# Kernel optimization log

Hardware: AMD Instinct MI355X
Metric: run time of the kernel (lower is better)

Reference implementation:

```python
import jax, jax.numpy as jnp
import numpy as np

N, E, IN, H, OUT, L = 100000, 1600000, 128, 64, 64, 3


def setup_inputs() -> dict:
    key = jax.random.key(0)
    ks = jax.random.split(key, 20)
    g = lambda i, shape: jax.random.normal(ks[i], shape, dtype=jnp.float32) * 0.05
    # architecture mixture weights: softmax of log_alpha ~ N(1, 0.01)
    sm = lambda i, rows, n: jax.nn.softmax(1.0 + 0.01 * jax.random.normal(ks[i], (rows, n), dtype=jnp.float32), axis=-1)
    return dict(
        x=jax.random.normal(ks[0], (N, IN), dtype=jnp.float32),
        edge_index=jax.random.randint(ks[1], (2, E), 0, N, dtype=jnp.int32),
        W_pre=g(2, (IN, H)), b_pre=jnp.zeros((H,), jnp.float32),
        W_self=g(3, (L, H, H)), b_self=jnp.zeros((L, H), jnp.float32),
        W_nbr=g(4, (L, H, H)), b_nbr=jnp.zeros((L, H), jnp.float32),
        W_comb=g(5, (L, 2 * H, H)), b_comb=jnp.zeros((L, H), jnp.float32),
        W_lc=g(6, (L, 2 * H, H)), b_lc=jnp.zeros((L, H), jnp.float32),
        ln_g=jnp.ones((L, H), jnp.float32), ln_b=jnp.zeros((L, H), jnp.float32),
        prelu_w=jnp.full((L,), 0.25, jnp.float32),
        W_lagg=g(7, ((L + 1) * H, H)), b_lagg=jnp.zeros((H,), jnp.float32),
        W_ff1=g(8, (H, H)), b_ff1=jnp.zeros((H,), jnp.float32),
        W_ff2=g(9, (H, OUT)), b_ff2=jnp.zeros((OUT,), jnp.float32),
        Z_agg=sm(10, L, 3), Z_comb=sm(11, L, 2), Z_act=sm(12, L, 2),
        Z_lc=sm(13, L, 3), Z_lagg=sm(14, 1, 3),
    )


def _layernorm(x, g, b, eps=1e-5):
    mu = x.mean(-1, keepdims=True)
    var = ((x - mu) ** 2).mean(-1, keepdims=True)
    return (x - mu) / jnp.sqrt(var + eps) * g + b


def reference(x, edge_index, W_pre, b_pre, W_self, b_self, W_nbr, b_nbr,
              W_comb, b_comb, W_lc, b_lc, ln_g, ln_b, prelu_w,
              W_lagg, b_lagg, W_ff1, b_ff1, W_ff2, b_ff2,
              Z_agg, Z_comb, Z_act, Z_lc, Z_lagg):
    n = x.shape[0]
    src, tgt = edge_index[0], edge_index[1]
    cnt = jax.ops.segment_sum(jnp.ones((src.shape[0], 1), x.dtype), tgt, num_segments=n)
    x = x @ W_pre + b_pre                       # preprocess: [N, H]
    embs = [x]
    for i in range(L):
        x_self = x @ W_self[i] + b_self[i]
        x_nl = x @ W_nbr[i] + b_nbr[i]
        msg = x_nl[src]                         # gather messages [E, H]
        s = jax.ops.segment_sum(msg, tgt, num_segments=n)
        mean = s / jnp.maximum(cnt, 1.0)
        mx = jax.ops.segment_max(msg, tgt, num_segments=n)
        mx = jnp.where(cnt > 0, mx, 0.0)        # empty segments -> 0 (PyG convention)
        x_n = Z_agg[i, 0] * s + Z_agg[i, 1] * mean + Z_agg[i, 2] * mx
        # combine mixture: sum / concat+merge
        c_sum = x_self + x_n
        c_cat = jnp.concatenate([x_self, x_n], -1) @ W_comb[i] + b_comb[i]
        h = Z_comb[i, 0] * c_sum + Z_comb[i, 1] * c_cat
        # act mixture: relu / prelu
        h = Z_act[i, 0] * jax.nn.relu(h) + Z_act[i, 1] * jnp.where(h > 0, h, prelu_w[i] * h)
        h = _layernorm(h, ln_g[i], ln_b[i])
        embs.append(h)
        # layer_connect mixture: stack / skip_sum / skip_cat
        lc_cat = jnp.concatenate([embs[-2], embs[-1]], -1) @ W_lc[i] + b_lc[i]
        x = Z_lc[i, 0] * h + Z_lc[i, 1] * (h + embs[-2]) + Z_lc[i, 2] * lc_cat
    # layer_agg mixture: none / max_pooling / concat+merge over emb_list
    a_none = embs[-1]
    a_max = jnp.stack(embs, 0).max(0)
    a_cat = jnp.concatenate(embs, -1) @ W_lagg + b_lagg
    out = Z_lagg[0, 0] * a_none + Z_lagg[0, 1] * a_max + Z_lagg[0, 2] * a_cat
    # feed-forward head (node-level task, no global pooling)
    out = jax.nn.relu(out @ W_ff1 + b_ff1) @ W_ff2 + b_ff2
    return out
```

## Files before the change

### kernel.cpp

```cpp
#include <hip/hip_runtime.h>

typedef unsigned short u16;
typedef unsigned int u32;
using bfrag = __attribute__((ext_vector_type(8))) short;
using f4v   = __attribute__((ext_vector_type(4))) float;

#define DIV_UP(a,b) (((a)+(b)-1)/(b))
#define PTILE 4096
#define CHB 512
#define CHSH 9
#define NBKT 256
#define MFMA(a,b,c) __builtin_amdgcn_mfma_f32_16x16x32_bf16(a,b,c,0,0,0)

__device__ inline u16 f2bf(float f){
  union { float f; u32 u; } v; v.f = f;
  u32 u = v.u;
  return (u16)((u + 0x7fffu + ((u >> 16) & 1u)) >> 16);
}
__device__ inline float bf2f(u16 h){
  union { u32 u; float f; } v; v.u = ((u32)h) << 16;
  return v.f;
}
__device__ inline bfrag ldA(const u16* A, long r, int koff, int lane){
  return *reinterpret_cast<const bfrag*>(A + r*64 + koff + ((lane>>4)<<3));
}
__device__ inline bfrag ldW(const u16* Wf, int kb, int cb, int lane){
  return *reinterpret_cast<const bfrag*>(Wf + (((kb*4+cb)*64 + lane)<<3));
}

__device__ inline void xpose_store(u16* sT, int lane, const f4v (&acc)[4]){
  const int cl = lane & 15, g = lane >> 4;
#pragma unroll
  for (int j = 0; j < 4; ++j){
    const int lr = g*4 + j;
#pragma unroll
    for (int cb = 0; cb < 4; ++cb){
      const int colblk = cb*2 + (cl >> 3);
      const int gr = colblk ^ (lr & 7);
      sT[lr*64 + gr*8 + (cl & 7)] = f2bf(acc[cb][j]);
    }
  }
}
__device__ inline bfrag xpose_load(const u16* sT, int lane, int kb){
  const int row = lane & 15, colblk = kb*4 + (lane >> 4);
  const int gr = colblk ^ (row & 7);
  return *reinterpret_cast<const bfrag*>(sT + row*64 + gr*8);
}

__global__ void initBkt_k(int* __restrict__ bktCnt, int bstride){
  if (threadIdx.x < NBKT) bktCnt[threadIdx.x] = threadIdx.x * bstride;
}
__global__ void partition_k(const int* __restrict__ tgt, const int* __restrict__ src,
                            int E, int* __restrict__ bktCnt, int2* __restrict__ bkt){
  __shared__ int hist[NBKT], base[NBKT], pos[NBKT];
  const int t = threadIdx.x;
  hist[t] = 0;
  __syncthreads();
  const int e0 = blockIdx.x * PTILE;
  const int e1 = (e0 + PTILE < E) ? e0 + PTILE : E;
  for (int i = e0 + t; i < e1; i += NBKT)
    atomicAdd(&hist[tgt[i] >> CHSH], 1);
  __syncthreads();
  base[t] = (hist[t] > 0) ? atomicAdd(&bktCnt[t], hist[t]) : 0;
  pos[t] = 0;
  __syncthreads();
  for (int i = e0 + t; i < e1; i += NBKT){
    int tv = tgt[i], sv = src[i];
    int c = tv >> CHSH;
    int p = base[c] + atomicAdd(&pos[c], 1);
    bkt[p] = make_int2(tv, sv);
  }
}

__global__ __launch_bounds__(CHB) void sortChunk_k(const int2* __restrict__ bkt,
    const int* __restrict__ bktCnt, int bstride, int N,
    int* __restrict__ cnt, int* __restrict__ off, int* __restrict__ perm){
  __shared__ int hist[CHB], sbase[CHB];
  const int c = blockIdx.x, t = threadIdx.x;
  const int lo = c * CHB;
  const int s = c * bstride, e = bktCnt[c];
  hist[t] = 0;
  __syncthreads();
  for (int i = s + t; i < e; i += CHB)
    atomicAdd(&hist[bkt[i].x - lo], 1);
  __syncthreads();
  const int v = hist[t];
  for (int o = 1; o < CHB; o <<= 1){
    int add = (t >= o) ? hist[t - o] : 0;
    __syncthreads();
    hist[t] += add;
    __syncthreads();
  }
  const int excl = hist[t] - v;
  if (lo + t < N){ cnt[lo + t] = v; off[lo + t] = s + excl; }
  sbase[t] = s + excl;
  __syncthreads();
  hist[t] = 0;
  __syncthreads();
  for (int i = s + t; i < e; i += CHB){
    int2 ed = bkt[i];
    int r = ed.x - lo;
    int p = sbase[r] + atomicAdd(&hist[r], 1);
    perm[p] = ed.y;
  }
}

__global__ void matW_k(const float* __restrict__ W_self, const float* __restrict__ W_comb,
                       const float* __restrict__ b_self,
                       float* __restrict__ WsWct, float* __restrict__ bsWct){
  const int b = blockIdx.x;
  const int i = b / 65, r = b % 65;
  const int c = threadIdx.x;
  const float* Wc = W_comb + i*8192;
  float s = 0.f;
  if (r < 64){
    const float* a = W_self + i*4096 + r*64;
#pragma unroll 8
    for (int k = 0; k < 64; ++k) s += a[k] * Wc[k*64 + c];
    WsWct[i*4096 + r*64 + c] = s;
  } else {
    const float* a = b_self + i*64;
#pragma unroll 8
    for (int k = 0; k < 64; ++k) s += a[k] * Wc[k*64 + c];
    bsWct[i*64 + c] = s;
  }
}

__global__ void buildAll_k(const float* __restrict__ W_self, const float* __restrict__ W_comb,
    const float* __restrict__ b_self, const float* __restrict__ b_comb,
    const float* __restrict__ Z_comb, const float* __restrict__ WsWct,
    const float* __restrict__ bsWct,
    const float* __restrict__ W_lc, const float* __restrict__ b_lc,
    const float* __restrict__ Z_lc,
    const float* __restrict__ W_lagg, const float* __restrict__ b_lagg,
    const float* __restrict__ Z_lagg,
    float* __restrict__ W1eff, float* __restrict__ W2eff, float* __restrict__ beff,
    float* __restrict__ Wlceff, float* __restrict__ blceff,
    float* __restrict__ Wle, float* __restrict__ ble){
  int idx = blockIdx.x*blockDim.x + threadIdx.x;
  if (idx < 12288){
    int i = idx >> 12, rem = idx & 4095, k = rem >> 6, c = rem & 63;
    float zc0 = Z_comb[i*2], zc1 = Z_comb[i*2+1];
    W1eff[idx] = zc0*W_self[idx] + zc1*WsWct[idx];
    W2eff[idx] = (k == c ? zc0 : 0.f) + zc1*W_comb[i*8192 + (64 + k)*64 + c];
    return;
  }
  idx -= 12288;
  if (idx < 16384){
    int i = idx >> 13, rem = idx & 8191, k = rem >> 6, c = rem & 63;
    float z0 = Z_lc[i*3], z1 = Z_lc[i*3+1], z2 = Z_lc[i*3+2];
    float idv = (k < 64) ? (k == c ? z1 : 0.f) : ((k - 64) == c ? (z0 + z1) : 0.f);
    Wlceff[idx] = z2*W_lc[idx] + idv;
    return;
  }
  idx -= 16384;
  if (idx < 20480){
    int k = idx >> 6, c = idx & 63;
    float v = (k < 256) ? Z_lagg[2]*W_lagg[idx] : 0.f;
    if (k >= 192 && k < 256 && (k - 192) == c) v += Z_lagg[0];
    if (k >= 256 && (k - 256) == c) v += Z_lagg[1];
    Wle[idx] = v;
    return;
  }
  idx -= 20480;
  if (idx < 192){
    int i = idx >> 6;
    float zc0 = Z_comb[i*2], zc1 = Z_comb[i*2+1];
    beff[idx] = zc0*b_self[idx] + zc1*(bsWct[idx] + b_comb[idx]);
    return;
  }
  idx -= 192;
  if (idx < 128){
    int i = idx >> 6;
    blceff[idx] = Z_lc[i*3+2]*b_lc[idx];
    return;
  }
  idx -= 128;
  if (idx < 64) ble[idx] = Z_lagg[2]*b_lagg[idx];
}

struct PackJobs {
  const float* src[15];
  u16* dst[15];
  int nkb[15];
};
__global__ void pack_all_k(PackJobs pj){
  const int job = blockIdx.x >> 4, kb = blockIdx.x & 15;
  if (kb >= pj.nkb[job]) return;
  const int t = threadIdx.x, cb = t >> 6, lane = t & 63;
  const float* S = pj.src[job];
  u16* D = pj.dst[job] + (((kb*4 + cb)*64 + lane) << 3);
  const int kbase = kb*32 + ((lane >> 4) << 3), c = cb*16 + (lane & 15);
#pragma unroll
  for (int j = 0; j < 8; ++j) D[j] = f2bf(S[(kbase + j)*64 + c]);
}

__global__ __launch_bounds__(256) void gemmP_k(const float* __restrict__ X,
    const u16* __restrict__ Wf, const float* __restrict__ bias,
    const u16* __restrict__ Wn, const float* __restrict__ bn,
    u16* __restrict__ out, u16* __restrict__ xnl, int N){
  __shared__ u16 sT[4][1024];
  const int lane = threadIdx.x & 63, w = threadIdx.x >> 6;
  const int R = blockIdx.x*64 + w*16;
  bfrag wf[4][4], wn[2][4];
#pragma unroll
  for (int kb = 0; kb < 4; ++kb)
#pragma unroll
    for (int cb = 0; cb < 4; ++cb) wf[kb][cb] = ldW(Wf, kb, cb, lane);
#pragma unroll
  for (int kb = 0; kb < 2; ++kb)
#pragma unroll
    for (int cb = 0; cb < 4; ++cb) wn[kb][cb] = ldW(Wn, kb, cb, lane);
  float bv[4], bnv[4];
#pragma unroll
  for (int cb = 0; cb < 4; ++cb){ bv[cb] = bias[cb*16 + (lane & 15)]; bnv[cb] = bn[cb*16 + (lane & 15)]; }
  const long ra = (R + (lane & 15) < N) ? (R + (lane & 15)) : (N - 1);
  f4v acc[4] = {f4v{0,0,0,0}, f4v{0,0,0,0}, f4v{0,0,0,0}, f4v{0,0,0,0}};
#pragma unroll
  for (int kb = 0; kb < 4; ++kb){
    const float* ap = X + ra*128 + kb*32 + ((lane >> 4) << 3);
    float4 q0 = *reinterpret_cast<const float4*>(ap);
    float4 q1 = *reinterpret_cast<const float4*>(ap + 4);
    bfrag a;
    a[0] = (short)f2bf(q0.x); a[1] = (short)f2bf(q0.y);
    a[2] = (short)f2bf(q0.z); a[3] = (short)f2bf(q0.w);
    a[4] = (short)f2bf(q1.x); a[5] = (short)f2bf(q1.y);
    a[6] = (short)f2bf(q1.z); a[7] = (short)f2bf(q1.w);
#pragma unroll
    for (int cb = 0; cb < 4; ++cb) acc[cb] = MFMA(a, wf[kb][cb], acc[cb]);
  }
#pragma unroll
  for (int cb = 0; cb < 4; ++cb)
#pragma unroll
    for (int j = 0; j < 4; ++j) acc[cb][j] += bv[cb];
  const int rbase = R + ((lane >> 4) << 2), cl = lane & 15;
#pragma unroll
  for (int cb = 0; cb < 4; ++cb)
#pragma unroll
    for (int j = 0; j < 4; ++j){
      int r = rbase + j;
      if (r < N) out[(size_t)r*64 + cb*16 + cl] = f2bf(acc[cb][j]);
    }
  xpose_store(sT[w], lane, acc);
  f4v ac2[4] = {f4v{0,0,0,0}, f4v{0,0,0,0}, f4v{0,0,0,0}, f4v{0,0,0,0}};
#pragma unroll
  for (int kb = 0; kb < 2; ++kb){
    bfrag a = xpose_load(sT[w], lane, kb);
#pragma unroll
    for (int cb = 0; cb < 4; ++cb) ac2[cb] = MFMA(a, wn[kb][cb], ac2[cb]);
  }
#pragma unroll
  for (int cb = 0; cb < 4; ++cb)
#pragma unroll
    for (int j = 0; j < 4; ++j){
      int r = rbase + j;
      if (r < N) xnl[(size_t)r*64 + cb*16 + cl] = f2bf(ac2[cb][j] + bnv[cb]);
    }
}

__global__ __launch_bounds__(256) void gemmC_k(const u16* __restrict__ A1,
    const u16* __restrict__ A2, const u16* __restrict__ Wf1, const u16* __restrict__ Wf2,
    const float* __restrict__ beff, const float* __restrict__ lng, const float* __restrict__ lnb,
    const float* __restrict__ Zact, const float* __restrict__ prelu,
    u16* __restrict__ out, int N){
  const int lane = threadIdx.x & 63, w = threadIdx.x >> 6;
  const int R = blockIdx.x*64 + w*16;
  bfrag wf1[2][4], wf2[2][4];
#pragma unroll
  for (int kb = 0; kb < 2; ++kb)
#pragma unroll
    for (int cb = 0; cb < 4; ++cb){ wf1[kb][cb] = ldW(Wf1, kb, cb, lane); wf2[kb][cb] = ldW(Wf2, kb, cb, lane); }
  float bv[4], lgv[4], lbv[4];
#pragma unroll
  for (int cb = 0; cb < 4; ++cb){
    int c = cb*16 + (lane & 15);
    bv[cb] = beff[c]; lgv[cb] = lng[c]; lbv[cb] = lnb[c];
  }
  const float zt0 = Zact[0], zt1 = Zact[1], pw = prelu[0];
  const long ra = (R + (lane & 15) < N) ? (R + (lane & 15)) : (N - 1);
  f4v acc[4] = {f4v{0,0,0,0}, f4v{0,0,0,0}, f4v{0,0,0,0}, f4v{0,0,0,0}};
#pragma unroll
  for (int kb = 0; kb < 2; ++kb){
    bfrag a = ldA(A1, ra, kb*32, lane);
#pragma unroll
    for (int cb = 0; cb < 4; ++cb) acc[cb] = MFMA(a, wf1[kb][cb], acc[cb]);
  }
#pragma unroll
  for (int kb = 0; kb < 2; ++kb){
    bfrag a = ldA(A2, ra, kb*32, lane);
#pragma unroll
    for (int cb = 0; cb < 4; ++cb) acc[cb] = MFMA(a, wf2[kb][cb], acc[cb]);
  }
#pragma unroll
  for (int cb = 0; cb < 4; ++cb)
#pragma unroll
    for (int j = 0; j < 4; ++j){
      float v = acc[cb][j] + bv[cb];
      v = zt0*fmaxf(v, 0.f) + zt1*((v > 0.f) ? v : pw*v);
      acc[cb][j] = v;
    }
  const int rbase = R + ((lane >> 4) << 2), cl = lane & 15;
#pragma unroll
  for (int j = 0; j < 4; ++j){
    float s = acc[0][j] + acc[1][j] + acc[2][j] + acc[3][j];
    s += __shfl_xor(s, 1, 64); s += __shfl_xor(s, 2, 64);
    s += __shfl_xor(s, 4, 64); s += __shfl_xor(s, 8, 64);
    float mu = s * 0.015625f;
    float d0 = acc[0][j]-mu, d1 = acc[1][j]-mu, d2 = acc[2][j]-mu, d3 = acc[3][j]-mu;
    float q = d0*d0 + d1*d1 + d2*d2 + d3*d3;
    q += __shfl_xor(q, 1, 64); q += __shfl_xor(q, 2, 64);
    q += __shfl_xor(q, 4, 64); q += __shfl_xor(q, 8, 64);
    float sd = rsqrtf(q * 0.015625f + 1e-5f);
    int r = rbase + j;
    if (r < N){
      out[(size_t)r*64 +  0 + cl] = f2bf(d0*sd*lgv[0] + lbv[0]);
      out[(size_t)r*64 + 16 + cl] = f2bf(d1*sd*lgv[1] + lbv[1]);
      out[(size_t)r*64 + 32 + cl] = f2bf(d2*sd*lgv[2] + lbv[2]);
      out[(size_t)r*64 + 48 + cl] = f2bf(d3*sd*lgv[3] + lbv[3]);
    }
  }
}

__global__ __launch_bounds__(256) void lc_k(const u16* __restrict__ A1,
    const u16* __restrict__ A2, const u16* __restrict__ Wf,
    const float* __restrict__ bias, const u16* __restrict__ Wn,
    const float* __restrict__ bn, u16* __restrict__ out, u16* __restrict__ xnl, int N){
  __shared__ u16 sT[4][1024];
  const int lane = threadIdx.x & 63, w = threadIdx.x >> 6;
  const int R = blockIdx.x*64 + w*16;
  bfrag wf[4][4], wn[2][4];
#pragma unroll
  for (int kb = 0; kb < 4; ++kb)
#pragma unroll
    for (int cb = 0; cb < 4; ++cb) wf[kb][cb] = ldW(Wf, kb, cb, lane);
#pragma unroll
  for (int kb = 0; kb < 2; ++kb)
#pragma unroll
    for (int cb = 0; cb < 4; ++cb) wn[kb][cb] = ldW(Wn, kb, cb, lane);
  float bv[4], bnv[4];
#pragma unroll
  for (int cb = 0; cb < 4; ++cb){ bv[cb] = bias[cb*16 + (lane & 15)]; bnv[cb] = bn[cb*16 + (lane & 15)]; }
  const long ra = (R + (lane & 15) < N) ? (R + (lane & 15)) : (N - 1);
  f4v acc[4] = {f4v{0,0,0,0}, f4v{0,0,0,0}, f4v{0,0,0,0}, f4v{0,0,0,0}};
#pragma unroll
  for (int kb = 0; kb < 4; ++kb){
    bfrag a = (kb < 2) ? ldA(A1, ra, kb*32, lane) : ldA(A2, ra, (kb-2)*32, lane);
#pragma unroll
    for (int cb = 0; cb < 4; ++cb) acc[cb] = MFMA(a, wf[kb][cb], acc[cb]);
  }
#pragma unroll
  for (int cb = 0; cb < 4; ++cb)
#pragma unroll
    for (int j = 0; j < 4; ++j) acc[cb][j] += bv[cb];
  const int rbase = R + ((lane >> 4) << 2), cl = lane & 15;
#pragma unroll
  for (int cb = 0; cb < 4; ++cb)
#pragma unroll
    for (int j = 0; j < 4; ++j){
      int r = rbase + j;
      if (r < N) out[(size_t)r*64 + cb*16 + cl] = f2bf(acc[cb][j]);
    }
  xpose_store(sT[w], lane, acc);
  f4v ac2[4] = {f4v{0,0,0,0}, f4v{0,0,0,0}, f4v{0,0,0,0}, f4v{0,0,0,0}};
#pragma unroll
  for (int kb = 0; kb < 2; ++kb){
    bfrag a = xpose_load(sT[w], lane, kb);
#pragma unroll
    for (int cb = 0; cb < 4; ++cb) ac2[cb] = MFMA(a, wn[kb][cb], ac2[cb]);
  }
#pragma unroll
  for (int cb = 0; cb < 4; ++cb)
#pragma unroll
    for (int j = 0; j < 4; ++j){
      int r = rbase + j;
      if (r < N) xnl[(size_t)r*64 + cb*16 + cl] = f2bf(ac2[cb][j] + bnv[cb]);
    }
}

__global__ __launch_bounds__(256) void gemmL_k(const u16* __restrict__ e0,
    const u16* __restrict__ e1, const u16* __restrict__ e2, const u16* __restrict__ e3,
    const u16* __restrict__ Wf, const float* __restrict__ bias,
    u16* __restrict__ out, int N){
  const int lane = threadIdx.x & 63, w = threadIdx.x >> 6;
  const int R = blockIdx.x*64 + w*16;
  const u16* Ab[4] = {e0, e1, e2, e3};
  bfrag wf[10][4];
#pragma unroll
  for (int kb = 0; kb < 10; ++kb)
#pragma unroll
    for (int cb = 0; cb < 4; ++cb) wf[kb][cb] = ldW(Wf, kb, cb, lane);
  float bv[4];
#pragma unroll
  for (int cb = 0; cb < 4; ++cb) bv[cb] = bias[cb*16 + (lane & 15)];
  const long ra = (R + (lane & 15) < N) ? (R + (lane & 15)) : (N - 1);
  bfrag ae[10];
#pragma unroll
  for (int kb = 0; kb < 8; ++kb) ae[kb] = ldA(Ab[kb >> 1], ra, (kb & 1)*32, lane);
#pragma unroll
  for (int h = 0; h < 2; ++h){
    bfrag m;
#pragma unroll
    for (int i = 0; i < 8; ++i){
      float v0 = bf2f((u16)ae[0+h][i]), v1 = bf2f((u16)ae[2+h][i]);
      float v2 = bf2f((u16)ae[4+h][i]), v3 = bf2f((u16)ae[6+h][i]);
      m[i] = (short)f2bf(fmaxf(fmaxf(v0, v1), fmaxf(v2, v3)));
    }
    ae[8+h] = m;
  }
  f4v acc[4] = {f4v{0,0,0,0}, f4v{0,0,0,0}, f4v{0,0,0,0}, f4v{0,0,0,0}};
#pragma unroll
  for (int kb = 0; kb < 10; ++kb){
#pragma unroll
    for (int cb = 0; cb < 4; ++cb) acc[cb] = MFMA(ae[kb], wf[kb][cb], acc[cb]);
  }
  const int rbase = R + ((lane >> 4) << 2), cl = lane & 15;
#pragma unroll
  for (int cb = 0; cb < 4; ++cb)
#pragma unroll
    for (int j = 0; j < 4; ++j){
      int r = rbase + j;
      if (r < N) out[(size_t)r*64 + cb*16 + cl] = f2bf(acc[cb][j] + bv[cb]);
    }
}

__global__ __launch_bounds__(256) void ff12_k(const u16* __restrict__ A,
    const u16* __restrict__ Wf1, const float* __restrict__ b1,
    const u16* __restrict__ Wf2, const float* __restrict__ b2,
    float* __restrict__ out, int N){
  __shared__ u16 sT[4][1024];
  const int lane = threadIdx.x & 63, w = threadIdx.x >> 6;
  const int R = blockIdx.x*64 + w*16;
  bfrag wf1[2][4], wf2[2][4];
#pragma unroll
  for (int kb = 0; kb < 2; ++kb)
#pragma unroll
    for (int cb = 0; cb < 4; ++cb){ wf1[kb][cb] = ldW(Wf1, kb, cb, lane); wf2[kb][cb] = ldW(Wf2, kb, cb, lane); }
  float bv1[4], bv2[4];
#pragma unroll
  for (int cb = 0; cb < 4; ++cb){ bv1[cb] = b1[cb*16 + (lane & 15)]; bv2[cb] = b2[cb*16 + (lane & 15)]; }
  const long ra = (R + (lane & 15) < N) ? (R + (lane & 15)) : (N - 1);
  f4v acc[4] = {f4v{0,0,0,0}, f4v{0,0,0,0}, f4v{0,0,0,0}, f4v{0,0,0,0}};
#pragma unroll
  for (int kb = 0; kb < 2; ++kb){
    bfrag a = ldA(A, ra, kb*32, lane);
#pragma unroll
    for (int cb = 0; cb < 4; ++cb) acc[cb] = MFMA(a, wf1[kb][cb], acc[cb]);
  }
#pragma unroll
  for (int cb = 0; cb < 4; ++cb)
#pragma unroll
    for (int j = 0; j < 4; ++j) acc[cb][j] = fmaxf(acc[cb][j] + bv1[cb], 0.f);
  xpose_store(sT[w], lane, acc);
  f4v ac2[4] = {f4v{0,0,0,0}, f4v{0,0,0,0}, f4v{0,0,0,0}, f4v{0,0,0,0}};
#pragma unroll
  for (int kb = 0; kb < 2; ++kb){
    bfrag a = xpose_load(sT[w], lane, kb);
#pragma unroll
    for (int cb = 0; cb < 4; ++cb) ac2[cb] = MFMA(a, wf2[kb][cb], ac2[cb]);
  }
  const int rbase = R + ((lane >> 4) << 2), cl = lane & 15;
#pragma unroll
  for (int cb = 0; cb < 4; ++cb)
#pragma unroll
    for (int j = 0; j < 4; ++j){
      int r = rbase + j;
      if (r < N) out[(size_t)r*64 + cb*16 + cl] = ac2[cb][j] + bv2[cb];
    }
}

__global__ __launch_bounds__(256) void gather_k(const u16* __restrict__ xnl,
    const int* __restrict__ off, const int* __restrict__ cnt, const int* __restrict__ perm,
    const float* __restrict__ Z_agg, int layer, u16* __restrict__ xn, int N){
  const int lane = threadIdx.x & 63, w = threadIdx.x >> 6;
  const int g = lane >> 3;
  const int q = lane & 7;
  const int gbase = lane & 56;
  const int r = blockIdx.x*32 + w*8 + g;
  const float za0 = Z_agg[layer*3+0], za1 = Z_agg[layer*3+1], za2 = Z_agg[layer*3+2];
  int e0 = 0, deg = 0;
  if (r < N){ e0 = off[r]; deg = cnt[r]; }
  const float NI = -3.402823466e38f;
  float s0=0.f,s1=0.f,s2=0.f,s3=0.f,s4=0.f,s5=0.f,s6=0.f,s7=0.f;
  float m0=NI,m1=NI,m2=NI,m3=NI,m4=NI,m5=NI,m6=NI,m7=NI;
  for (int base = 0; base < deg; base += 8){
    int pe = (base + q < deg) ? perm[e0 + base + q] : 0;
    int nrem = deg - base; if (nrem > 8) nrem = 8;
#pragma unroll
    for (int j = 0; j < 8; ++j){
      if (j < nrem){
        int s = __shfl(pe, gbase + j, 64);
        uint4 u = reinterpret_cast<const uint4*>(xnl + ((size_t)s << 6))[q];
        float a0 = __uint_as_float(u.x << 16), a1 = __uint_as_float(u.x & 0xffff0000u);
        float a2 = __uint_as_float(u.y << 16), a3 = __uint_as_float(u.y & 0xffff0000u);
        float a4 = __uint_as_float(u.z << 16), a5 = __uint_as_float(u.z & 0xffff0000u);
        float a6 = __uint_as_float(u.w << 16), a7 = __uint_as_float(u.w & 0xffff0000u);
        s0 += a0; s1 += a1; s2 += a2; s3 += a3;
        s4 += a4; s5 += a5; s6 += a6; s7 += a7;
        m0 = fmaxf(m0, a0); m1 = fmaxf(m1, a1); m2 = fmaxf(m2, a2); m3 = fmaxf(m3, a3);
        m4 = fmaxf(m4, a4); m5 = fmaxf(m5, a5); m6 = fmaxf(m6, a6); m7 = fmaxf(m7, a7);
      }
    }
  }
  if (r < N){
    const float inv = 1.f / fmaxf((float)deg, 1.f);
    const float gz = (deg > 0) ? 1.f : 0.f;
    const float ca = za0 + za1*inv, cm = za2*gz;
    uint4 o;
    o.x = (u32)f2bf(ca*s0 + cm*m0) | (((u32)f2bf(ca*s1 + cm*m1)) << 16);
    o.y = (u32)f2bf(ca*s2 + cm*m2) | (((u32)f2bf(ca*s3 + cm*m3)) << 16);
    o.z = (u32)f2bf(ca*s4 + cm*m4) | (((u32)f2bf(ca*s5 + cm*m5)) << 16);
    o.w = (u32)f2bf(ca*s6 + cm*m6) | (((u32)f2bf(ca*s7 + cm*m7)) << 16);
    reinterpret_cast<uint4*>(xn + ((size_t)r << 6))[q] = o;
  }
}

extern "C" void kernel_launch(void* const* d_in, const int* in_sizes, int n_in,
                              void* d_out, int out_size, void* d_ws, size_t ws_size,
                              hipStream_t stream){
  const float* x      = (const float*)d_in[0];
  const int*   ei     = (const int*)  d_in[1];
  const float* W_pre  = (const float*)d_in[2];
  const float* b_pre  = (const float*)d_in[3];
  const float* W_self = (const float*)d_in[4];
  const float* b_self = (const float*)d_in[5];
  const float* W_nbr  = (const float*)d_in[6];
  const float* b_nbr  = (const float*)d_in[7];
  const float* W_comb = (const float*)d_in[8];
  const float* b_comb = (const float*)d_in[9];
  const float* W_lc   = (const float*)d_in[10];
  const float* b_lc   = (const float*)d_in[11];
  const float* ln_g   = (const float*)d_in[12];
  const float* ln_b   = (const float*)d_in[13];
  const float* prelu  = (const float*)d_in[14];
  const float* W_lagg = (const float*)d_in[15];
  const float* b_lagg = (const float*)d_in[16];
  const float* W_ff1  = (const float*)d_in[17];
  const float* b_ff1  = (const float*)d_in[18];
  const float* W_ff2  = (const float*)d_in[19];
  const float* b_ff2  = (const float*)d_in[20];
  const float* Z_agg  = (const float*)d_in[21];
  const float* Z_comb = (const float*)d_in[22];
  const float* Z_act  = (const float*)d_in[23];
  const float* Z_lc   = (const float*)d_in[24];
  const float* Z_lagg = (const float*)d_in[25];

  const int N = in_sizes[0] / 128;
  const int E = in_sizes[1] / 2;
  const int* src = ei;
  const int* tgt = ei + E;

  const int nch = DIV_UP(N, CHB);
  const int bstride = (int)(((long)E * CHB) / N) + 2048;

  char* p = (char*)d_ws;
  auto carve = [&](size_t bytes)->void*{
    void* q = (void*)p;
    p += (bytes + 255) & ~(size_t)255;
    return q;
  };
  int* cnt_i = (int*)carve((size_t)N*4);
  int* off   = (int*)carve((size_t)N*4);
  int* bktCnt= (int*)carve(NBKT*4);
  int2* bkt  = (int2*)carve((size_t)NBKT*bstride*8);
  int* perm  = (int*)carve((size_t)NBKT*bstride*4);
  float* WsWct = (float*)carve(3*4096*4);
  float* bsWct = (float*)carve(3*64*4);
  float* W1eff = (float*)carve(3*4096*4);
  float* W2eff = (float*)carve(3*4096*4);
  float* beff  = (float*)carve(3*64*4);
  float* Wlceff= (float*)carve(2*8192*4);
  float* blceff= (float*)carve(2*64*4);
  float* Wle   = (float*)carve(20480*4);
  float* ble   = (float*)carve(64*4);
  u16* pWpre = (u16*)carve(8192*2);
  u16* pWnbr = (u16*)carve(3*4096*2);
  u16* pW1   = (u16*)carve(3*4096*2);
  u16* pW2   = (u16*)carve(3*4096*2);
  u16* pWlc  = (u16*)carve(2*8192*2);
  u16* pWlagg= (u16*)carve(20480*2);
  u16* pWff1 = (u16*)carve(4096*2);
  u16* pWff2 = (u16*)carve(4096*2);
  const size_t AB = (size_t)N*64*2;
  u16* emb0 = (u16*)carve(AB);
  u16* emb1 = (u16*)carve(AB);
  u16* emb2 = (u16*)carve(AB);
  u16* emb3 = (u16*)carve(AB);
  u16* xbuf = (u16*)carve(AB);
  u16* xnl  = (u16*)carve(AB);
  u16* xn   = (u16*)carve(AB);
  u16* mixb = (u16*)carve(AB);

  initBkt_k<<<1,NBKT,0,stream>>>(bktCnt, bstride);
  partition_k<<<DIV_UP(E,PTILE),NBKT,0,stream>>>(tgt, src, E, bktCnt, bkt);
  sortChunk_k<<<nch,CHB,0,stream>>>(bkt, bktCnt, bstride, N, cnt_i, off, perm);

  matW_k<<<3*65,64,0,stream>>>(W_self, W_comb, b_self, WsWct, bsWct);
  buildAll_k<<<DIV_UP(49536,256),256,0,stream>>>(W_self, W_comb, b_self, b_comb, Z_comb,
                                                 WsWct, bsWct, W_lc, b_lc, Z_lc,
                                                 W_lagg, b_lagg, Z_lagg,
                                                 W1eff, W2eff, beff, Wlceff, blceff, Wle, ble);

  PackJobs pj;
  pj.src[0] = W_pre;  pj.dst[0] = pWpre;  pj.nkb[0] = 4;
  for (int i = 0; i < 3; ++i){
    pj.src[1+i] = W_nbr + i*4096; pj.dst[1+i] = pWnbr + i*4096; pj.nkb[1+i] = 2;
    pj.src[4+i] = W1eff + i*4096; pj.dst[4+i] = pW1   + i*4096; pj.nkb[4+i] = 2;
    pj.src[7+i] = W2eff + i*4096; pj.dst[7+i] = pW2   + i*4096; pj.nkb[7+i] = 2;
  }
  pj.src[10] = Wlceff;        pj.dst[10] = pWlc;        pj.nkb[10] = 4;
  pj.src[11] = Wlceff + 8192; pj.dst[11] = pWlc + 8192; pj.nkb[11] = 4;
  pj.src[12] = Wle;   pj.dst[12] = pWlagg; pj.nkb[12] = 10;
  pj.src[13] = W_ff1; pj.dst[13] = pWff1;  pj.nkb[13] = 2;
  pj.src[14] = W_ff2; pj.dst[14] = pWff2;  pj.nkb[14] = 2;
  pack_all_k<<<15*16,256,0,stream>>>(pj);

  const int G64 = DIV_UP(N, 64);

  gemmP_k<<<G64,256,0,stream>>>(x, pWpre, b_pre, pWnbr, b_nbr, emb0, xnl, N);

  u16* embs[4] = {emb0, emb1, emb2, emb3};
  const u16* xin = emb0;
  for (int i = 0; i < 3; ++i){
    gather_k<<<DIV_UP(N,32),256,0,stream>>>(xnl, off, cnt_i, perm, Z_agg, i, xn, N);
    gemmC_k<<<G64,256,0,stream>>>(xin, xn, pW1 + i*4096, pW2 + i*4096,
                                  beff + i*64, ln_g + i*64, ln_b + i*64,
                                  Z_act + i*2, prelu + i, embs[i+1], N);
    if (i < 2){
      lc_k<<<G64,256,0,stream>>>(embs[i], embs[i+1], pWlc + i*8192, blceff + i*64,
                                 pWnbr + (i+1)*4096, b_nbr + (i+1)*64, xbuf, xnl, N);
      xin = xbuf;
    }
  }

  gemmL_k<<<G64,256,0,stream>>>(emb0, emb1, emb2, emb3, pWlagg, ble, mixb, N);
  ff12_k<<<G64,256,0,stream>>>(mixb, pWff1, b_ff1, pWff2, b_ff2, (float*)d_out, N);
}
```

Before: 285.9 us.

## Process two nodes per gather group and stream weights in layer-agg GEMM

The gather kernel now has each 8-lane group handle two target nodes, interleaving their neighbor loads so more independent memory requests are in flight per wave, and the grid is halved to match. The layer-aggregation GEMM no longer preloads all 40 weight fragments and 10 activation fragments into registers. It streams them per k-block and builds the max-pool fragment incrementally, cutting register pressure to raise occupancy. The cost is more divergence in the gather when the two nodes' degrees differ, and per-iteration weight loads in the GEMM.

```diff
diff --git a/kernel.cpp b/kernel.cpp
--- a/kernel.cpp
+++ b/kernel.cpp
@@ -384,35 +384,29 @@
   const int lane = threadIdx.x & 63, w = threadIdx.x >> 6;
   const int R = blockIdx.x*64 + w*16;
   const u16* Ab[4] = {e0, e1, e2, e3};
-  bfrag wf[10][4];
-#pragma unroll
-  for (int kb = 0; kb < 10; ++kb)
-#pragma unroll
-    for (int cb = 0; cb < 4; ++cb) wf[kb][cb] = ldW(Wf, kb, cb, lane);
   float bv[4];
 #pragma unroll
   for (int cb = 0; cb < 4; ++cb) bv[cb] = bias[cb*16 + (lane & 15)];
   const long ra = (R + (lane & 15) < N) ? (R + (lane & 15)) : (N - 1);
-  bfrag ae[10];
-#pragma unroll
-  for (int kb = 0; kb < 8; ++kb) ae[kb] = ldA(Ab[kb >> 1], ra, (kb & 1)*32, lane);
-#pragma unroll
-  for (int h = 0; h < 2; ++h){
-    bfrag m;
-#pragma unroll
-    for (int i = 0; i < 8; ++i){
-      float v0 = bf2f((u16)ae[0+h][i]), v1 = bf2f((u16)ae[2+h][i]);
-      float v2 = bf2f((u16)ae[4+h][i]), v3 = bf2f((u16)ae[6+h][i]);
-      m[i] = (short)f2bf(fmaxf(fmaxf(v0, v1), fmaxf(v2, v3)));
-    }
-    ae[8+h] = m;
-  }
   f4v acc[4] = {f4v{0,0,0,0}, f4v{0,0,0,0}, f4v{0,0,0,0}, f4v{0,0,0,0}};
-#pragma unroll
-  for (int kb = 0; kb < 10; ++kb){
-#pragma unroll
-    for (int cb = 0; cb < 4; ++cb) acc[cb] = MFMA(ae[kb], wf[kb][cb], acc[cb]);
-  }
+  bfrag mx[2];
+#pragma unroll
+  for (int kb = 0; kb < 8; ++kb){
+    bfrag a = ldA(Ab[kb >> 1], ra, (kb & 1)*32, lane);
+    if (kb < 2){ mx[kb] = a; }
+    else {
+      bfrag& m = mx[kb & 1];
+#pragma unroll
+      for (int i = 0; i < 8; ++i)
+        m[i] = (short)f2bf(fmaxf(bf2f((u16)m[i]), bf2f((u16)a[i])));
+    }
+#pragma unroll
+    for (int cb = 0; cb < 4; ++cb) acc[cb] = MFMA(a, ldW(Wf, kb, cb, lane), acc[cb]);
+  }
+#pragma unroll
+  for (int kb = 8; kb < 10; ++kb)
+#pragma unroll
+    for (int cb = 0; cb < 4; ++cb) acc[cb] = MFMA(mx[kb-8], ldW(Wf, kb, cb, lane), acc[cb]);
   const int rbase = R + ((lane >> 4) << 2), cl = lane & 15;
 #pragma unroll
   for (int cb = 0; cb < 4; ++cb)
@@ -475,42 +469,71 @@
   const int g = lane >> 3;
   const int q = lane & 7;
   const int gbase = lane & 56;
-  const int r = blockIdx.x*32 + w*8 + g;
+  const int rA = blockIdx.x*64 + w*16 + g;
+  const int rB = rA + 8;
   const float za0 = Z_agg[layer*3+0], za1 = Z_agg[layer*3+1], za2 = Z_agg[layer*3+2];
-  int e0 = 0, deg = 0;
-  if (r < N){ e0 = off[r]; deg = cnt[r]; }
+  int eA = 0, dA = 0, eB = 0, dB = 0;
+  if (rA < N){ eA = off[rA]; dA = cnt[rA]; }
+  if (rB < N){ eB = off[rB]; dB = cnt[rB]; }
   const float NI = -3.402823466e38f;
-  float s0=0.f,s1=0.f,s2=0.f,s3=0.f,s4=0.f,s5=0.f,s6=0.f,s7=0.f;
-  float m0=NI,m1=NI,m2=NI,m3=NI,m4=NI,m5=NI,m6=NI,m7=NI;
-  for (int base = 0; base < deg; base += 8){
-    int pe = (base + q < deg) ? perm[e0 + base + q] : 0;
-    int nrem = deg - base; if (nrem > 8) nrem = 8;
+  float sA0=0.f,sA1=0.f,sA2=0.f,sA3=0.f,sA4=0.f,sA5=0.f,sA6=0.f,sA7=0.f;
+  float mA0=NI,mA1=NI,mA2=NI,mA3=NI,mA4=NI,mA5=NI,mA6=NI,mA7=NI;
+  float sB0=0.f,sB1=0.f,sB2=0.f,sB3=0.f,sB4=0.f,sB5=0.f,sB6=0.f,sB7=0.f;
+  float mB0=NI,mB1=NI,mB2=NI,mB3=NI,mB4=NI,mB5=NI,mB6=NI,mB7=NI;
+  const u16* xq = xnl + q*8;
+  const int dmax = (dA > dB) ? dA : dB;
+  for (int base = 0; base < dmax; base += 8){
+    int peA = (base + q < dA) ? perm[eA + base + q] : 0;
+    int peB = (base + q < dB) ? perm[eB + base + q] : 0;
 #pragma unroll
     for (int j = 0; j < 8; ++j){
-      if (j < nrem){
-        int s = __shfl(pe, gbase + j, 64);
-        uint4 u = reinterpret_cast<const uint4*>(xnl + ((size_t)s << 6))[q];
+      int sAi = __shfl(peA, gbase + j, 64);
+      int sBi = __shfl(peB, gbase + j, 64);
+      if (base + j < dA){
+        uint4 u = *reinterpret_cast<const uint4*>(xq + ((size_t)sAi << 6));
         float a0 = __uint_as_float(u.x << 16), a1 = __uint_as_float(u.x & 0xffff0000u);
         float a2 = __uint_as_float(u.y << 16), a3 = __uint_as_float(u.y & 0xffff0000u);
         float a4 = __uint_as_float(u.z << 16), a5 = __uint_as_float(u.z & 0xffff0000u);
         float a6 = __uint_as_float(u.w << 16), a7 = __uint_as_float(u.w & 0xffff0000u);
-        s0 += a0; s1 += a1; s2 += a2; s3 += a3;
-        s4 += a4; s5 += a5; s6 += a6; s7 += a7;
-        m0 = fmaxf(m0, a0); m1 = fmaxf(m1, a1); m2 = fmaxf(m2, a2); m3 = fmaxf(m3, a3);
-        m4 = fmaxf(m4, a4); m5 = fmaxf(m5, a5); m6 = fmaxf(m6, a6); m7 = fmaxf(m7, a7);
+        sA0 += a0; sA1 += a1; sA2 += a2; sA3 += a3;
+        sA4 += a4; sA5 += a5; sA6 += a6; sA7 += a7;
+        mA0 = fmaxf(mA0, a0); mA1 = fmaxf(mA1, a1); mA2 = fmaxf(mA2, a2); mA3 = fmaxf(mA3, a3);
+        mA4 = fmaxf(mA4, a4); mA5 = fmaxf(mA5, a5); mA6 = fmaxf(mA6, a6); mA7 = fmaxf(mA7, a7);
       }
-    }
-  }
-  if (r < N){
-    const float inv = 1.f / fmaxf((float)deg, 1.f);
-    const float gz = (deg > 0) ? 1.f : 0.f;
+      if (base + j < dB){
+        uint4 u = *reinterpret_cast<const uint4*>(xq + ((size_t)sBi << 6));
+        float a0 = __uint_as_float(u.x << 16), a1 = __uint_as_float(u.x & 0xffff0000u);
+        float a2 = __uint_as_float(u.y << 16), a3 = __uint_as_float(u.y & 0xffff0000u);
+        float a4 = __uint_as_float(u.z << 16), a5 = __uint_as_float(u.z & 0xffff0000u);
+        float a6 = __uint_as_float(u.w << 16), a7 = __uint_as_float(u.w & 0xffff0000u);
+        sB0 += a0; sB1 += a1; sB2 += a2; sB3 += a3;
+        sB4 += a4; sB5 += a5; sB6 += a6; sB7 += a7;
+        mB0 = fmaxf(mB0, a0); mB1 = fmaxf(mB1, a1); mB2 = fmaxf(mB2, a2); mB3 = fmaxf(mB3, a3);
+        mB4 = fmaxf(mB4, a4); mB5 = fmaxf(mB5, a5); mB6 = fmaxf(mB6, a6); mB7 = fmaxf(mB7, a7);
+      }
+    }
+  }
+  if (rA < N){
+    const float inv = 1.f / fmaxf((float)dA, 1.f);
+    const float gz = (dA > 0) ? 1.f : 0.f;
     const float ca = za0 + za1*inv, cm = za2*gz;
     uint4 o;
-    o.x = (u32)f2bf(ca*s0 + cm*m0) | (((u32)f2bf(ca*s1 + cm*m1)) << 16);
-    o.y = (u32)f2bf(ca*s2 + cm*m2) | (((u32)f2bf(ca*s3 + cm*m3)) << 16);
-    o.z = (u32)f2bf(ca*s4 + cm*m4) | (((u32)f2bf(ca*s5 + cm*m5)) << 16);
-    o.w = (u32)f2bf(ca*s6 + cm*m6) | (((u32)f2bf(ca*s7 + cm*m7)) << 16);
-    reinterpret_cast<uint4*>(xn + ((size_t)r << 6))[q] = o;
+    o.x = (u32)f2bf(ca*sA0 + cm*mA0) | (((u32)f2bf(ca*sA1 + cm*mA1)) << 16);
+    o.y = (u32)f2bf(ca*sA2 + cm*mA2) | (((u32)f2bf(ca*sA3 + cm*mA3)) << 16);
+    o.z = (u32)f2bf(ca*sA4 + cm*mA4) | (((u32)f2bf(ca*sA5 + cm*mA5)) << 16);
+    o.w = (u32)f2bf(ca*sA6 + cm*mA6) | (((u32)f2bf(ca*sA7 + cm*mA7)) << 16);
+    reinterpret_cast<uint4*>(xn + ((size_t)rA << 6))[q] = o;
+  }
+  if (rB < N){
+    const float inv = 1.f / fmaxf((float)dB, 1.f);
+    const float gz = (dB > 0) ? 1.f : 0.f;
+    const float ca = za0 + za1*inv, cm = za2*gz;
+    uint4 o;
+    o.x = (u32)f2bf(ca*sB0 + cm*mB0) | (((u32)f2bf(ca*sB1 + cm*mB1)) << 16);
+    o.y = (u32)f2bf(ca*sB2 + cm*mB2) | (((u32)f2bf(ca*sB3 + cm*mB3)) << 16);
+    o.z = (u32)f2bf(ca*sB4 + cm*mB4) | (((u32)f2bf(ca*sB5 + cm*mB5)) << 16);
+    o.w = (u32)f2bf(ca*sB6 + cm*mB6) | (((u32)f2bf(ca*sB7 + cm*mB7)) << 16);
+    reinterpret_cast<uint4*>(xn + ((size_t)rB << 6))[q] = o;
   }
 }
 
@@ -621,7 +644,7 @@
   u16* embs[4] = {emb0, emb1, emb2, emb3};
   const u16* xin = emb0;
   for (int i = 0; i < 3; ++i){
-    gather_k<<<DIV_UP(N,32),256,0,stream>>>(xnl, off, cnt_i, perm, Z_agg, i, xn, N);
+    gather_k<<<G64,256,0,stream>>>(xnl, off, cnt_i, perm, Z_agg, i, xn, N);
     gemmC_k<<<G64,256,0,stream>>>(xin, xn, pW1 + i*4096, pW2 + i*4096,
                                   beff + i*64, ln_g + i*64, ln_b + i*64,
                                   Z_act + i*2, prelu + i, embs[i+1], N);
```

Result: no change. 289.3 us (+1.2%).

## Fuse combine and layer-connect kernels, batch gather loads, stream gemmL weights

Applied to the files above, without the earlier changes.

Merges the per-layer combine/activation/LayerNorm kernel with the layer-connect and next-layer neighbour GEMM into one kernel for the first two layers. This removes one launch per layer and the re-read of the freshly written embedding from global memory. The gather kernel now prefetches the next batch of edge indices and issues all eight row loads before accumulating, to raise memory-level parallelism. The tail loads for short rows fetch a dummy row, which costs some extra traffic. The layer-aggregation GEMM streams its weights and computes the running max incrementally instead of holding forty weight fragments in registers, which lowers register pressure.

```diff
diff --git a/kernel.cpp b/kernel.cpp
--- a/kernel.cpp
+++ b/kernel.cpp
@@ -321,59 +321,109 @@
   }
 }
 
-__global__ __launch_bounds__(256) void lc_k(const u16* __restrict__ A1,
-    const u16* __restrict__ A2, const u16* __restrict__ Wf,
-    const float* __restrict__ bias, const u16* __restrict__ Wn,
-    const float* __restrict__ bn, u16* __restrict__ out, u16* __restrict__ xnl, int N){
+__global__ __launch_bounds__(256) void gemmCL_k(const u16* __restrict__ A1,
+    const u16* __restrict__ A2, const u16* __restrict__ Aprev,
+    const u16* __restrict__ Wf1, const u16* __restrict__ Wf2,
+    const float* __restrict__ beff, const float* __restrict__ lng, const float* __restrict__ lnb,
+    const float* __restrict__ Zact, const float* __restrict__ prelu,
+    const u16* __restrict__ Wlc, const float* __restrict__ blc,
+    const u16* __restrict__ Wn, const float* __restrict__ bn,
+    u16* __restrict__ emb_out, u16* __restrict__ x_out, u16* __restrict__ xnl, int N){
   __shared__ u16 sT[4][1024];
   const int lane = threadIdx.x & 63, w = threadIdx.x >> 6;
   const int R = blockIdx.x*64 + w*16;
-  bfrag wf[4][4], wn[2][4];
-#pragma unroll
-  for (int kb = 0; kb < 4; ++kb)
-#pragma unroll
-    for (int cb = 0; cb < 4; ++cb) wf[kb][cb] = ldW(Wf, kb, cb, lane);
+  bfrag wf1[2][4], wf2[2][4];
 #pragma unroll
   for (int kb = 0; kb < 2; ++kb)
 #pragma unroll
-    for (int cb = 0; cb < 4; ++cb) wn[kb][cb] = ldW(Wn, kb, cb, lane);
-  float bv[4], bnv[4];
-#pragma unroll
-  for (int cb = 0; cb < 4; ++cb){ bv[cb] = bias[cb*16 + (lane & 15)]; bnv[cb] = bn[cb*16 + (lane & 15)]; }
+    for (int cb = 0; cb < 4; ++cb){ wf1[kb][cb] = ldW(Wf1, kb, cb, lane); wf2[kb][cb] = ldW(Wf2, kb, cb, lane); }
+  float bv[4], lgv[4], lbv[4], blcv[4], bnv[4];
+#pragma unroll
+  for (int cb = 0; cb < 4; ++cb){
+    int c = cb*16 + (lane & 15);
+    bv[cb] = beff[c]; lgv[cb] = lng[c]; lbv[cb] = lnb[c];
+    blcv[cb] = blc[c]; bnv[cb] = bn[c];
+  }
+  const float zt0 = Zact[0], zt1 = Zact[1], pw = prelu[0];
   const long ra = (R + (lane & 15) < N) ? (R + (lane & 15)) : (N - 1);
   f4v acc[4] = {f4v{0,0,0,0}, f4v{0,0,0,0}, f4v{0,0,0,0}, f4v{0,0,0,0}};
 #pragma unroll
-  for (int kb = 0; kb < 4; ++kb){
-    bfrag a = (kb < 2) ? ldA(A1, ra, kb*32, lane) : ldA(A2, ra, (kb-2)*32, lane);
-#pragma unroll
-    for (int cb = 0; cb < 4; ++cb) acc[cb] = MFMA(a, wf[kb][cb], acc[cb]);
-  }
-#pragma unroll
-  for (int cb = 0; cb < 4; ++cb)
-#pragma unroll
-    for (int j = 0; j < 4; ++j) acc[cb][j] += bv[cb];
+  for (int kb = 0; kb < 2; ++kb){
+    bfrag a = ldA(A1, ra, kb*32, lane);
+#pragma unroll
+    for (int cb = 0; cb < 4; ++cb) acc[cb] = MFMA(a, wf1[kb][cb], acc[cb]);
+  }
+#pragma unroll
+  for (int kb = 0; kb < 2; ++kb){
+    bfrag a = ldA(A2, ra, kb*32, lane);
+#pragma unroll
+    for (int cb = 0; cb < 4; ++cb) acc[cb] = MFMA(a, wf2[kb][cb], acc[cb]);
+  }
+#pragma unroll
+  for (int cb = 0; cb < 4; ++cb)
+#pragma unroll
+    for (int j = 0; j < 4; ++j){
+      float v = acc[cb][j] + bv[cb];
+      v = zt0*fmaxf(v, 0.f) + zt1*((v > 0.f) ? v : pw*v);
+      acc[cb][j] = v;
+    }
   const int rbase = R + ((lane >> 4) << 2), cl = lane & 15;
 #pragma unroll
-  for (int cb = 0; cb < 4; ++cb)
-#pragma unroll
-    for (int j = 0; j < 4; ++j){
-      int r = rbase + j;
-      if (r < N) out[(size_t)r*64 + cb*16 + cl] = f2bf(acc[cb][j]);
-    }
+  for (int j = 0; j < 4; ++j){
+    float s = acc[0][j] + acc[1][j] + acc[2][j] + acc[3][j];
+    s += __shfl_xor(s, 1, 64); s += __shfl_xor(s, 2, 64);
+    s += __shfl_xor(s, 4, 64); s += __shfl_xor(s, 8, 64);
+    float mu = s * 0.015625f;
+    float d0 = acc[0][j]-mu, d1 = acc[1][j]-mu, d2 = acc[2][j]-mu, d3 = acc[3][j]-mu;
+    float q = d0*d0 + d1*d1 + d2*d2 + d3*d3;
+    q += __shfl_xor(q, 1, 64); q += __shfl_xor(q, 2, 64);
+    q += __shfl_xor(q, 4, 64); q += __shfl_xor(q, 8, 64);
+    float sd = rsqrtf(q * 0.015625f + 1e-5f);
+    acc[0][j] = d0*sd*lgv[0] + lbv[0];
+    acc[1][j] = d1*sd*lgv[1] + lbv[1];
+    acc[2][j] = d2*sd*lgv[2] + lbv[2];
+    acc[3][j] = d3*sd*lgv[3] + lbv[3];
+    int r = rbase + j;
+    if (r < N){
+      emb_out[(size_t)r*64 +  0 + cl] = f2bf(acc[0][j]);
+      emb_out[(size_t)r*64 + 16 + cl] = f2bf(acc[1][j]);
+      emb_out[(size_t)r*64 + 32 + cl] = f2bf(acc[2][j]);
+      emb_out[(size_t)r*64 + 48 + cl] = f2bf(acc[3][j]);
+    }
+  }
   xpose_store(sT[w], lane, acc);
   f4v ac2[4] = {f4v{0,0,0,0}, f4v{0,0,0,0}, f4v{0,0,0,0}, f4v{0,0,0,0}};
 #pragma unroll
+  for (int kb = 0; kb < 4; ++kb){
+    bfrag a = (kb < 2) ? ldA(Aprev, ra, kb*32, lane) : xpose_load(sT[w], lane, kb - 2);
+#pragma unroll
+    for (int cb = 0; cb < 4; ++cb) ac2[cb] = MFMA(a, ldW(Wlc, kb, cb, lane), ac2[cb]);
+  }
+#pragma unroll
+  for (int cb = 0; cb < 4; ++cb)
+#pragma unroll
+    for (int j = 0; j < 4; ++j) ac2[cb][j] += blcv[cb];
+#pragma unroll
+  for (int cb = 0; cb < 4; ++cb)
+#pragma unroll
+    for (int j = 0; j < 4; ++j){
+      int r = rbase + j;
+      if (r < N) x_out[(size_t)r*64 + cb*16 + cl] = f2bf(ac2[cb][j]);
+    }
+  xpose_store(sT[w], lane, ac2);
+  f4v ac3[4] = {f4v{0,0,0,0}, f4v{0,0,0,0}, f4v{0,0,0,0}, f4v{0,0,0,0}};
+#pragma unroll
   for (int kb = 0; kb < 2; ++kb){
     bfrag a = xpose_load(sT[w], lane, kb);
 #pragma unroll
-    for (int cb = 0; cb < 4; ++cb) ac2[cb] = MFMA(a, wn[kb][cb], ac2[cb]);
+    for (int cb = 0; cb < 4; ++cb) ac3[cb] = MFMA(a, ldW(Wn, kb, cb, lane), ac3[cb]);
   }
 #pragma unroll
   for (int cb = 0; cb < 4; ++cb)
 #pragma unroll
     for (int j = 0; j < 4; ++j){
       int r = rbase + j;
-      if (r < N) xnl[(size_t)r*64 + cb*16 + cl] = f2bf(ac2[cb][j] + bnv[cb]);
+      if (r < N) xnl[(size_t)r*64 + cb*16 + cl] = f2bf(ac3[cb][j] + bnv[cb]);
     }
 }
 
@@ -384,35 +434,29 @@
   const int lane = threadIdx.x & 63, w = threadIdx.x >> 6;
   const int R = blockIdx.x*64 + w*16;
   const u16* Ab[4] = {e0, e1, e2, e3};
-  bfrag wf[10][4];
-#pragma unroll
-  for (int kb = 0; kb < 10; ++kb)
-#pragma unroll
-    for (int cb = 0; cb < 4; ++cb) wf[kb][cb] = ldW(Wf, kb, cb, lane);
   float bv[4];
 #pragma unroll
   for (int cb = 0; cb < 4; ++cb) bv[cb] = bias[cb*16 + (lane & 15)];
   const long ra = (R + (lane & 15) < N) ? (R + (lane & 15)) : (N - 1);
-  bfrag ae[10];
-#pragma unroll
-  for (int kb = 0; kb < 8; ++kb) ae[kb] = ldA(Ab[kb >> 1], ra, (kb & 1)*32, lane);
-#pragma unroll
-  for (int h = 0; h < 2; ++h){
-    bfrag m;
-#pragma unroll
-    for (int i = 0; i < 8; ++i){
-      float v0 = bf2f((u16)ae[0+h][i]), v1 = bf2f((u16)ae[2+h][i]);
-      float v2 = bf2f((u16)ae[4+h][i]), v3 = bf2f((u16)ae[6+h][i]);
-      m[i] = (short)f2bf(fmaxf(fmaxf(v0, v1), fmaxf(v2, v3)));
-    }
-    ae[8+h] = m;
-  }
   f4v acc[4] = {f4v{0,0,0,0}, f4v{0,0,0,0}, f4v{0,0,0,0}, f4v{0,0,0,0}};
-#pragma unroll
-  for (int kb = 0; kb < 10; ++kb){
-#pragma unroll
-    for (int cb = 0; cb < 4; ++cb) acc[cb] = MFMA(ae[kb], wf[kb][cb], acc[cb]);
-  }
+  bfrag mx[2];
+#pragma unroll
+  for (int kb = 0; kb < 8; ++kb){
+    bfrag a = ldA(Ab[kb >> 1], ra, (kb & 1)*32, lane);
+    if (kb < 2){ mx[kb] = a; }
+    else {
+      bfrag& m = mx[kb & 1];
+#pragma unroll
+      for (int i = 0; i < 8; ++i)
+        m[i] = (short)f2bf(fmaxf(bf2f((u16)m[i]), bf2f((u16)a[i])));
+    }
+#pragma unroll
+    for (int cb = 0; cb < 4; ++cb) acc[cb] = MFMA(a, ldW(Wf, kb, cb, lane), acc[cb]);
+  }
+#pragma unroll
+  for (int kb = 8; kb < 10; ++kb)
+#pragma unroll
+    for (int cb = 0; cb < 4; ++cb) acc[cb] = MFMA(mx[kb-8], ldW(Wf, kb, cb, lane), acc[cb]);
   const int rbase = R + ((lane >> 4) << 2), cl = lane & 15;
 #pragma unroll
   for (int cb = 0; cb < 4; ++cb)
@@ -482,14 +526,21 @@
   const float NI = -3.402823466e38f;
   float s0=0.f,s1=0.f,s2=0.f,s3=0.f,s4=0.f,s5=0.f,s6=0.f,s7=0.f;
   float m0=NI,m1=NI,m2=NI,m3=NI,m4=NI,m5=NI,m6=NI,m7=NI;
+  const u16* xq = xnl + q*8;
+  int pe = (q < deg) ? perm[e0 + q] : 0;
   for (int base = 0; base < deg; base += 8){
-    int pe = (base + q < deg) ? perm[e0 + base + q] : 0;
-    int nrem = deg - base; if (nrem > 8) nrem = 8;
+    int pe_n = (base + 8 + q < deg) ? perm[e0 + base + 8 + q] : 0;
+    int idx[8];
+#pragma unroll
+    for (int j = 0; j < 8; ++j) idx[j] = __shfl(pe, gbase + j, 64);
+    uint4 ub[8];
+#pragma unroll
+    for (int j = 0; j < 8; ++j)
+      ub[j] = *reinterpret_cast<const uint4*>(xq + ((size_t)idx[j] << 6));
 #pragma unroll
     for (int j = 0; j < 8; ++j){
-      if (j < nrem){
-        int s = __shfl(pe, gbase + j, 64);
-        uint4 u = reinterpret_cast<const uint4*>(xnl + ((size_t)s << 6))[q];
+      if (base + j < deg){
+        uint4 u = ub[j];
         float a0 = __uint_as_float(u.x << 16), a1 = __uint_as_float(u.x & 0xffff0000u);
         float a2 = __uint_as_float(u.y << 16), a3 = __uint_as_float(u.y & 0xffff0000u);
         float a4 = __uint_as_float(u.z << 16), a5 = __uint_as_float(u.z & 0xffff0000u);
@@ -500,6 +551,7 @@
         m4 = fmaxf(m4, a4); m5 = fmaxf(m5, a5); m6 = fmaxf(m6, a6); m7 = fmaxf(m7, a7);
       }
     }
+    pe = pe_n;
   }
   if (r < N){
     const float inv = 1.f / fmaxf((float)deg, 1.f);
@@ -622,13 +674,19 @@
   const u16* xin = emb0;
   for (int i = 0; i < 3; ++i){
     gather_k<<<DIV_UP(N,32),256,0,stream>>>(xnl, off, cnt_i, perm, Z_agg, i, xn, N);
-    gemmC_k<<<G64,256,0,stream>>>(xin, xn, pW1 + i*4096, pW2 + i*4096,
-                                  beff + i*64, ln_g + i*64, ln_b + i*64,
-                                  Z_act + i*2, prelu + i, embs[i+1], N);
     if (i < 2){
-      lc_k<<<G64,256,0,stream>>>(embs[i], embs[i+1], pWlc + i*8192, blceff + i*64,
-                                 pWnbr + (i+1)*4096, b_nbr + (i+1)*64, xbuf, xnl, N);
+      gemmCL_k<<<G64,256,0,stream>>>(xin, xn, embs[i],
+                                     pW1 + i*4096, pW2 + i*4096,
+                                     beff + i*64, ln_g + i*64, ln_b + i*64,
+                                     Z_act + i*2, prelu + i,
+                                     pWlc + i*8192, blceff + i*64,
+                                     pWnbr + (i+1)*4096, b_nbr + (i+1)*64,
+                                     embs[i+1], xbuf, xnl, N);
       xin = xbuf;
+    } else {
+      gemmC_k<<<G64,256,0,stream>>>(xin, xn, pW1 + i*4096, pW2 + i*4096,
+                                    beff + i*64, ln_g + i*64, ln_b + i*64,
+                                    Z_act + i*2, prelu + i, embs[i+1], N);
     }
   }
 
```

Result: faster. 268.5 us (-6.1%).
